# Kernel optimization log

Hardware: AMD Instinct MI355X
Metric: run time of the kernel (lower is better)

The kernel has to match this reference:

```python
import jax, jax.numpy as jnp
import numpy as np

N = 4096
D = 1024
NUM_INSTANCES = 8  # samples per class; classes = N // NUM_INSTANCES
MARGIN = 0.5


def setup_inputs() -> dict:
    key = jax.random.key(0)
    x = jax.random.normal(key, (N, D), dtype=jnp.float32)
    # L2-normalize embeddings so dot products are cosine sims in [-1, 1]
    x = x / jnp.linalg.norm(x, axis=1, keepdims=True)
    targets = (jnp.arange(N) // NUM_INSTANCES).astype(jnp.int64)
    return {"inputs": x, "targets": targets}


def reference(inputs, targets):
    # Faithful to the torch module with mean=False. The per-row Python loop
    # with sort + masked_select reduces to: sum over positive pairs of (1 - sim)
    # plus sum over negative pairs of sim where sim > margin, divided by n.
    # (The sort is irrelevant under a sum reduction.)
    n = inputs.shape[0]
    sim = inputs @ inputs.T                      # [n, n]
    same = targets[:, None] == targets[None, :]  # [n, n] bool
    eye = jnp.eye(n, dtype=bool)
    pos_mask = same & ~eye
    neg_mask = ~same
    pos_loss = jnp.sum(jnp.where(pos_mask, 1.0 - sim, 0.0))
    neg_loss = jnp.sum(jnp.where(neg_mask & (sim > MARGIN), sim, 0.0))
    return (pos_loss + neg_loss) / n
```

## Files before the change

### kernel.cpp

```cpp
#include <hip/hip_runtime.h>
#include <hip/hip_bf16.h>
#include <stdint.h>


#define NROWS 4096
#define DDIM  1024
#define BT    256
#define BK    64
#define GT    (NROWS / BT)
#define NT    (DDIM / BK)
#define HT    (128 * 64)
#define MARGIN 0.5f

typedef __attribute__((ext_vector_type(8)))  short  bf16x8;
typedef __attribute__((ext_vector_type(16))) float  f32x16;
typedef __attribute__((ext_vector_type(8)))  unsigned short u16x8;

#define AS1 __attribute__((address_space(1)))
#define AS3 __attribute__((address_space(3)))

#define BAR()    asm volatile("s_barrier" ::: "memory")
#define SCHEDB() __builtin_amdgcn_sched_barrier(0)

__device__ __forceinline__ unsigned short f2bf(float f) {
    unsigned u = __float_as_uint(f);
    u += 0x7FFFu + ((u >> 16) & 1u);
    return (unsigned short)(u >> 16);
}

__global__ void convert_kernel(const float* __restrict__ x,
                               unsigned short* __restrict__ xb,
                               float* __restrict__ out) {
    int i = blockIdx.x * blockDim.x + threadIdx.x;
    if (i == 0) out[0] = 0.0f;
    float4 v0 = ((const float4*)x)[2 * i];
    float4 v1 = ((const float4*)x)[2 * i + 1];
    u16x8 o;
    o[0] = f2bf(v0.x); o[1] = f2bf(v0.y); o[2] = f2bf(v0.z); o[3] = f2bf(v0.w);
    o[4] = f2bf(v1.x); o[5] = f2bf(v1.y); o[6] = f2bf(v1.z); o[7] = f2bf(v1.w);
    ((u16x8*)xb)[i] = o;
}

__global__ __launch_bounds__(512, 2)
void pairloss_kernel(const unsigned short* __restrict__ xb,
                     float* __restrict__ out) {
    __shared__ __attribute__((aligned(16))) unsigned short lds[2][4][HT];
    __shared__ float wsum[8];

    const int x = blockIdx.x & 7, w = blockIdx.x >> 3;
    const int s = (x << 1) | (w >> 4);
    const int bi = ((s >> 2) << 2) | ((w >> 2) & 3);
    const int bj = ((s & 3) << 2) | (w & 3);
    const int Ra = bi * BT, Rb = bj * BT;

    const int tid  = threadIdx.x;
    const int lane = tid & 63;
    const int wid  = tid >> 6;
    const int wr = wid >> 2;
    const int wc = wid & 3;
    const int r32 = lane & 31;
    const int kh  = lane >> 5;

    const int ha = wr;
    const int hb = 2 + (wc >> 1);
    const int rbo = (wc & 1) * 64;

    f32x16 acc[4][2] = {};

    auto stage_half = [&](int b, int h, int T) {
        const int R0 = ((h < 2) ? Ra : Rb) + (h & 1) * 128;
        #pragma unroll
        for (int q = 0; q < 2; ++q) {
            int l = q * 512 + tid;
            int r = l >> 3;
            int sc = (l & 7) ^ (r & 7);
            __builtin_amdgcn_global_load_lds(
                (AS1 void*)(xb + (size_t)(R0 + r) * DDIM + T * BK + sc * 8),
                (AS3 void*)(&lds[b][h][l * 8]), 16, 0, 0);
        }
    };
    auto stage_tile = [&](int b, int T) {
        stage_half(b, 0, T); stage_half(b, 1, T);
        stage_half(b, 2, T); stage_half(b, 3, T);
    };

    stage_tile(0, 0);
    stage_tile(1, 1);

    for (int t = 0; t < NT; ++t) {
        const int b = t & 1;
        if (t < NT - 1) asm volatile("s_waitcnt vmcnt(8)" ::: "memory");
        else            asm volatile("s_waitcnt vmcnt(0)" ::: "memory");
        BAR();
        SCHEDB();

        #pragma unroll
        for (int kk = 0; kk < 4; ++kk) {
            const int ch = ((kk * 2 + kh) ^ (lane & 7)) * 8;
            bf16x8 af[4], bfr[2];
            #pragma unroll
            for (int rb = 0; rb < 4; ++rb)
                af[rb] = *(const bf16x8*)&lds[b][ha][(rb * 32 + r32) * 64 + ch];
            #pragma unroll
            for (int cb = 0; cb < 2; ++cb)
                bfr[cb] = *(const bf16x8*)&lds[b][hb][(rbo + cb * 32 + r32) * 64 + ch];
            __builtin_amdgcn_s_setprio(1);
            #pragma unroll
            for (int rb = 0; rb < 4; ++rb)
                #pragma unroll
                for (int cb = 0; cb < 2; ++cb)
                    acc[rb][cb] = __builtin_amdgcn_mfma_f32_32x32x16_bf16(
                        af[rb], bfr[cb], acc[rb][cb], 0, 0, 0);
            __builtin_amdgcn_s_setprio(0);
        }
        SCHEDB();
        BAR();
        if (t + 2 < NT) stage_tile(b, t + 2);
    }

    float part = 0.f;
    #pragma unroll
    for (int rb = 0; rb < 4; ++rb) {
        #pragma unroll
        for (int cb = 0; cb < 2; ++cb) {
            #pragma unroll
            for (int reg = 0; reg < 16; ++reg) {
                float sv = acc[rb][cb][reg];
                int row = (reg & 3) + 8 * (reg >> 2) + 4 * kh;
                int i = Ra + wr * 128 + rb * 32 + row;
                int j = Rb + wc * 64  + cb * 32 + r32;
                bool same = ((i >> 3) == (j >> 3));
                float c = same ? ((i == j) ? 0.f : (1.f - sv))
                               : ((sv > MARGIN) ? sv : 0.f);
                part += c;
            }
        }
    }
    part *= (1.f / NROWS);

    #pragma unroll
    for (int off = 32; off > 0; off >>= 1)
        part += __shfl_down(part, off, 64);
    if (lane == 0) wsum[wid] = part;
    __syncthreads();
    if (tid == 0) {
        float ssum = 0.f;
        #pragma unroll
        for (int wv = 0; wv < 8; ++wv) ssum += wsum[wv];
        atomicAdd(out, ssum);
    }
}

extern "C" void kernel_launch(void* const* d_in, const int* in_sizes, int n_in,
                              void* d_out, int out_size, void* d_ws, size_t ws_size,
                              hipStream_t stream) {
    const float* xin = (const float*)d_in[0];
    float* out = (float*)d_out;
    unsigned short* xb = (unsigned short*)d_ws;

    convert_kernel<<<(NROWS * DDIM / 8) / 256, 256, 0, stream>>>(xin, xb, out);
    pairloss_kernel<<<GT * GT, 512, 0, stream>>>(xb, out);
}
```

Before: 104.3 us.

## Switch similarity GEMM from bf16 to scaled fp8 MFMA

```diff
diff --git a/kernel.cpp b/kernel.cpp
--- a/kernel.cpp
+++ b/kernel.cpp
@@ -6,15 +6,15 @@
 #define NROWS 4096
 #define DDIM  1024
 #define BT    256
-#define BK    64
+#define BK    128
 #define GT    (NROWS / BT)
 #define NT    (DDIM / BK)
-#define HT    (128 * 64)
+#define HB    (128 * 128)
 #define MARGIN 0.5f
 
-typedef __attribute__((ext_vector_type(8)))  short  bf16x8;
+typedef __attribute__((ext_vector_type(8)))  int    i32x8;
+typedef __attribute__((ext_vector_type(4)))  int    i32x4;
 typedef __attribute__((ext_vector_type(16))) float  f32x16;
-typedef __attribute__((ext_vector_type(8)))  unsigned short u16x8;
 
 #define AS1 __attribute__((address_space(1)))
 #define AS3 __attribute__((address_space(3)))
@@ -22,29 +22,36 @@
 #define BAR()    asm volatile("s_barrier" ::: "memory")
 #define SCHEDB() __builtin_amdgcn_sched_barrier(0)
 
-__device__ __forceinline__ unsigned short f2bf(float f) {
-    unsigned u = __float_as_uint(f);
-    u += 0x7FFFu + ((u >> 16) & 1u);
-    return (unsigned short)(u >> 16);
-}
-
 __global__ void convert_kernel(const float* __restrict__ x,
-                               unsigned short* __restrict__ xb,
+                               unsigned int* __restrict__ x8,
                                float* __restrict__ out) {
     int i = blockIdx.x * blockDim.x + threadIdx.x;
     if (i == 0) out[0] = 0.0f;
     float4 v0 = ((const float4*)x)[2 * i];
     float4 v1 = ((const float4*)x)[2 * i + 1];
-    u16x8 o;
-    o[0] = f2bf(v0.x); o[1] = f2bf(v0.y); o[2] = f2bf(v0.z); o[3] = f2bf(v0.w);
-    o[4] = f2bf(v1.x); o[5] = f2bf(v1.y); o[6] = f2bf(v1.z); o[7] = f2bf(v1.w);
-    ((u16x8*)xb)[i] = o;
+    const float S = 32.0f;
+    int w0 = __builtin_amdgcn_cvt_pk_fp8_f32(v0.x * S, v0.y * S, 0, false);
+    w0     = __builtin_amdgcn_cvt_pk_fp8_f32(v0.z * S, v0.w * S, w0, true);
+    int w1 = __builtin_amdgcn_cvt_pk_fp8_f32(v1.x * S, v1.y * S, 0, false);
+    w1     = __builtin_amdgcn_cvt_pk_fp8_f32(v1.z * S, v1.w * S, w1, true);
+    x8[2 * i]     = (unsigned int)w0;
+    x8[2 * i + 1] = (unsigned int)w1;
+}
+
+__device__ __forceinline__ i32x8 ld_frag(const unsigned char* hbase, int row,
+                                         int c0, int s8) {
+    i32x4 lo = *(const i32x4*)(hbase + row * BK + (((c0)     ^ s8) * 16));
+    i32x4 hi = *(const i32x4*)(hbase + row * BK + (((c0 + 1) ^ s8) * 16));
+    i32x8 r;
+    r[0] = lo[0]; r[1] = lo[1]; r[2] = lo[2]; r[3] = lo[3];
+    r[4] = hi[0]; r[5] = hi[1]; r[6] = hi[2]; r[7] = hi[3];
+    return r;
 }
 
 __global__ __launch_bounds__(512, 2)
-void pairloss_kernel(const unsigned short* __restrict__ xb,
+void pairloss_kernel(const unsigned char* __restrict__ x8,
                      float* __restrict__ out) {
-    __shared__ __attribute__((aligned(16))) unsigned short lds[2][4][HT];
+    __shared__ __attribute__((aligned(16))) unsigned char lds8[2][4][HB];
     __shared__ float wsum[8];
 
     const int x = blockIdx.x & 7, w = blockIdx.x >> 3;
@@ -60,6 +67,7 @@
     const int wc = wid & 3;
     const int r32 = lane & 31;
     const int kh  = lane >> 5;
+    const int s8  = r32 & 7;
 
     const int ha = wr;
     const int hb = 2 + (wc >> 1);
@@ -75,8 +83,8 @@
             int r = l >> 3;
             int sc = (l & 7) ^ (r & 7);
             __builtin_amdgcn_global_load_lds(
-                (AS1 void*)(xb + (size_t)(R0 + r) * DDIM + T * BK + sc * 8),
-                (AS3 void*)(&lds[b][h][l * 8]), 16, 0, 0);
+                (AS1 void*)(x8 + (size_t)(R0 + r) * DDIM + T * BK + sc * 16),
+                (AS3 void*)(&lds8[b][h][l * 16]), 16, 0, 0);
         }
     };
     auto stage_tile = [&](int b, int T) {
@@ -95,22 +103,25 @@
         SCHEDB();
 
         #pragma unroll
-        for (int kk = 0; kk < 4; ++kk) {
-            const int ch = ((kk * 2 + kh) ^ (lane & 7)) * 8;
-            bf16x8 af[4], bfr[2];
+        for (int st = 0; st < 2; ++st) {
+            const int c0 = st * 4 + kh * 2;
+            i32x8 af[4], bfr[2];
             #pragma unroll
             for (int rb = 0; rb < 4; ++rb)
-                af[rb] = *(const bf16x8*)&lds[b][ha][(rb * 32 + r32) * 64 + ch];
+                af[rb] = ld_frag(&lds8[b][ha][0], rb * 32 + r32, c0, s8);
             #pragma unroll
             for (int cb = 0; cb < 2; ++cb)
-                bfr[cb] = *(const bf16x8*)&lds[b][hb][(rbo + cb * 32 + r32) * 64 + ch];
+                bfr[cb] = ld_frag(&lds8[b][hb][0], rbo + cb * 32 + r32, c0, s8);
             __builtin_amdgcn_s_setprio(1);
             #pragma unroll
             for (int rb = 0; rb < 4; ++rb)
                 #pragma unroll
                 for (int cb = 0; cb < 2; ++cb)
-                    acc[rb][cb] = __builtin_amdgcn_mfma_f32_32x32x16_bf16(
-                        af[rb], bfr[cb], acc[rb][cb], 0, 0, 0);
+                    acc[rb][cb] = __builtin_amdgcn_mfma_scale_f32_32x32x64_f8f6f4(
+                        af[rb], bfr[cb], acc[rb][cb],
+                        0, 0,
+                        0, 0x7F7F7F7Fu,
+                        0, 0x7F7F7F7Fu);
             __builtin_amdgcn_s_setprio(0);
         }
         SCHEDB();
@@ -125,7 +136,7 @@
         for (int cb = 0; cb < 2; ++cb) {
             #pragma unroll
             for (int reg = 0; reg < 16; ++reg) {
-                float sv = acc[rb][cb][reg];
+                float sv = acc[rb][cb][reg] * 0.0009765625f;
                 int row = (reg & 3) + 8 * (reg >> 2) + 4 * kh;
                 int i = Ra + wr * 128 + rb * 32 + row;
                 int j = Rb + wc * 64  + cb * 32 + r32;
@@ -156,8 +167,9 @@
                               hipStream_t stream) {
     const float* xin = (const float*)d_in[0];
     float* out = (float*)d_out;
-    unsigned short* xb = (unsigned short*)d_ws;
+    unsigned int* x8w = (unsigned int*)d_ws;
+    const unsigned char* x8r = (const unsigned char*)d_ws;
 
-    convert_kernel<<<(NROWS * DDIM / 8) / 256, 256, 0, stream>>>(xin, xb, out);
-    pairloss_kernel<<<GT * GT, 512, 0, stream>>>(xb, out);
+    convert_kernel<<<(NROWS * DDIM / 8) / 256, 256, 0, stream>>>(xin, x8w, out);
+    pairloss_kernel<<<GT * GT, 512, 0, stream>>>(x8r, out);
 }
```

Measured after the change: 270.7 us. 159% more time.
